# Performance work log

Measured on AMD Instinct MI355X. Metric: run time of the kernel, lower is better.

Reference implementation:

```python
import jax, jax.numpy as jnp
import numpy as np

WL = 5.32e-7      # wavelength (m)
DX = 8e-6         # pixel size (m)
N = 128           # image_size
L_COH = 2e-4      # coherence length used for training screens
DISTANCES = [0.0795, 0.0795, 0.106, 0.106]  # 3 inter-layer props + final prop (repeats last)


def _freq_grids():
    fx = jnp.fft.fftfreq(N, DX).astype(jnp.float32)
    FX, FY = jnp.meshgrid(fx, fx)  # 'xy' indexing, matches np.meshgrid default
    return FX, FY


def _prop_kernels():
    # Angular-spectrum transfer functions H(fx,fy) = exp(i*kz*z), evanescent cut.
    FX, FY = _freq_grids()
    k = 2.0 * np.pi / WL
    k2 = FX ** 2 + FY ** 2
    valid = (k2 <= (1.0 / WL) ** 2).astype(jnp.float32)
    kz = jnp.sqrt(jnp.maximum(k * k - k2 * valid, 0.0)) * valid
    return jnp.stack([jnp.exp(1j * kz * z) for z in DISTANCES]).astype(jnp.complex64)  # (4,N,N)


def _screens(c_noise):
    # Gaussian-Schell random screens T_m = fftshift(ifft2(C_m * sqrt(p(v)))) * H * W
    FX, FY = _freq_grids()
    v = jnp.sqrt(FX ** 2 + FY ** 2)
    p_v = 2.0 * np.pi * L_COH ** 2 * jnp.exp(-2.0 * (np.pi * L_COH * v) ** 2)
    C = (c_noise[..., 0] + 1j * c_noise[..., 1]).astype(jnp.complex64)  # (M,N,N)
    F_T = C * jnp.sqrt(p_v + 1e-12).astype(jnp.complex64)
    T = jnp.fft.fftshift(jnp.fft.ifft2(F_T), axes=(-2, -1)) * (N * N)
    return T  # (M,N,N) complex64


def setup_inputs() -> dict:
    key = jax.random.key(0)
    k1, k2, k3 = jax.random.split(key, 3)
    B, M = 32, 100
    x_in = jax.random.uniform(k1, (B, N, N), dtype=jnp.float32)
    phases = jax.random.uniform(k2, (3, N, N), dtype=jnp.float32) * (2.0 * np.pi)
    c_noise = jax.random.normal(k3, (M, N, N, 2), dtype=jnp.float32)
    return {"x_in": x_in, "phases": phases, "c_noise": c_noise, "M": M}


def reference(x_in, phases, c_noise, M):
    Hs = _prop_kernels()                # (4,N,N)
    T = _screens(c_noise[:M])           # (M,N,N)
    # field: (M,B,N,N) complex64 -- Monte-Carlo axis fully vectorized
    field = x_in.astype(jnp.complex64)[None, :, :, :] * T[:, None, :, :]
    for j in range(3):
        field = jnp.fft.ifft2(jnp.fft.fft2(field) * Hs[j])
        field = field * jnp.exp(1j * phases[j]).astype(jnp.complex64)
    field = jnp.fft.ifft2(jnp.fft.fft2(field) * Hs[3])
    intensity = jnp.sum(jnp.abs(field) ** 2, axis=(-2, -1))  # (M,B)
    return jnp.mean(intensity, axis=0)  # (B,)
```

## Files before the change

kernel.cpp:

```cpp
#include <hip/hip_runtime.h>
#include <hip/hip_fp16.h>


struct cplx { float x, y; };
__device__ __forceinline__ cplx cadd(cplx a, cplx b){ return {a.x+b.x, a.y+b.y}; }
__device__ __forceinline__ cplx csub(cplx a, cplx b){ return {a.x-b.x, a.y-b.y}; }
__device__ __forceinline__ cplx cmul(cplx a, cplx b){ return {a.x*b.x - a.y*b.y, a.x*b.y + a.y*b.x}; }
__device__ __forceinline__ cplx cmuli(cplx a){ return {-a.y, a.x}; }

__device__ __forceinline__ void idft4(cplx&A,cplx&B,cplx&C,cplx&D){
    cplx e0=cadd(A,C), e1=csub(A,C), o0=cadd(B,D), o1=csub(B,D);
    cplx i1 = cmuli(o1);
    A=cadd(e0,o0); B=cadd(e1,i1); C=csub(e0,o0); D=csub(e1,i1);
}
__device__ __forceinline__ void idft8(cplx a[8]){
    cplx e0=a[0],e1=a[2],e2=a[4],e3=a[6];
    cplx o0=a[1],o1=a[3],o2=a[5],o3=a[7];
    idft4(e0,e1,e2,e3); idft4(o0,o1,o2,o3);
    const float Ch = 0.70710678118654752f;
    cplx t1 = cmul(o1, cplx{ Ch, Ch});
    cplx t2 = cmuli(o2);
    cplx t3 = cmul(o3, cplx{-Ch, Ch});
    a[0]=cadd(e0,o0); a[4]=csub(e0,o0);
    a[1]=cadd(e1,t1); a[5]=csub(e1,t1);
    a[2]=cadd(e2,t2); a[6]=csub(e2,t2);
    a[3]=cadd(e3,t3); a[7]=csub(e3,t3);
}
__device__ __forceinline__ void idft16(cplx a[16]){
    cplx e[8]={a[0],a[2],a[4],a[6],a[8],a[10],a[12],a[14]};
    cplx o[8]={a[1],a[3],a[5],a[7],a[9],a[11],a[13],a[15]};
    idft8(e); idft8(o);
    const float Ch=0.70710678118654752f, c1=0.92387953251128674f, s1=0.38268343236508977f;
    const cplx w[8]={{1.f,0.f},{c1,s1},{Ch,Ch},{s1,c1},{0.f,1.f},{-s1,c1},{-Ch,Ch},{-c1,s1}};
    #pragma unroll
    for(int n=0;n<8;++n){ cplx t=cmul(o[n],w[n]); a[n]=cadd(e[n],t); a[n+8]=csub(e[n],t); }
}

#define LDSP 130
#define NR   16
#define MG   2

__device__ __forceinline__ void fft128_rows(cplx* fld, const cplx* tw, int tid)
{
    const int r = tid >> 3, t = tid & 7;
    cplx* row = fld + r * LDSP;
    {   cplx a[16];
        #pragma unroll
        for (int k1 = 0; k1 < 16; ++k1) a[k1] = row[t + 8*k1];
        idft16(a);
        #pragma unroll
        for (int n1 = 0; n1 < 16; ++n1) row[t + 8*n1] = cmul(a[n1], tw[(n1*t) & 127]);
    }
    __syncthreads();
    {   cplx b0[8], b1[8];
        #pragma unroll
        for (int k2 = 0; k2 < 8; ++k2) { b0[k2] = row[8*t + k2]; b1[k2] = row[8*(t+8) + k2]; }
        idft8(b0); idft8(b1);
        __syncthreads();
        #pragma unroll
        for (int n2 = 0; n2 < 8; ++n2) {
            row[ t      + 16*n2] = b0[n2];
            row[(t + 8) + 16*n2] = b1[n2];
        }
    }
    __syncthreads();
}

__device__ __forceinline__ unsigned h2_to_u(__half2 h){
    union { __half2 h; unsigned u; } v; v.h = h; return v.u;
}

__global__ __launch_bounds__(128)
void rowfft_kernel(const float* __restrict__ c_noise, __half2* __restrict__ mid,
                   float* __restrict__ Wsh)
{
    __shared__ cplx fld[NR * LDSP];
    __shared__ cplx tw[128];
    const int m   = blockIdx.x;
    const int rb  = blockIdx.y * NR;
    const int tid = threadIdx.x;

    if (m == 0) {
        float4* wz = (float4*)Wsh;
        #pragma unroll
        for (int k = 0; k < 4; ++k)
            wz[blockIdx.y*512 + k*128 + tid] = {0.f, 0.f, 0.f, 0.f};
    }

    {   float s, c;
        sincosf((float)tid * (float)(2.0 * M_PI / 128.0), &s, &c);
        tw[tid] = { c, s };
    }

    const float DF = 976.5625f;
    const float Ac = 2.5132741228718345e-7f;
    const float Bc = 7.8956835208714865e-7f;
    #pragma unroll
    for (int it = 0; it < NR; ++it) {
        const int i = rb + it, j = tid;
        float fi = (float)(((i+64)&127) - 64) * DF;
        float fj = (float)(((j+64)&127) - 64) * DF;
        float G  = sqrtf(Ac * expf(-Bc * (fi*fi + fj*fj)) + 1e-12f);
        float2 cv = ((const float2*)c_noise)[(size_t)m*16384 + i*128 + j];
        fld[it*LDSP + j] = { cv.x * G, cv.y * G };
    }
    __syncthreads();

    fft128_rows(fld, tw, tid);

    const int c = tid;
    uint4* dst4 = (uint4*)(mid + (size_t)m*16384 + (size_t)c*128 + rb);
    #pragma unroll
    for (int q = 0; q < 4; ++q) {
        uint4 pk;
        cplx v0 = fld[(4*q+0)*LDSP + c];
        cplx v1 = fld[(4*q+1)*LDSP + c];
        cplx v2 = fld[(4*q+2)*LDSP + c];
        cplx v3 = fld[(4*q+3)*LDSP + c];
        pk.x = h2_to_u(__floats2half2_rn(v0.x, v0.y));
        pk.y = h2_to_u(__floats2half2_rn(v1.x, v1.y));
        pk.z = h2_to_u(__floats2half2_rn(v2.x, v2.y));
        pk.w = h2_to_u(__floats2half2_rn(v3.x, v3.y));
        dst4[q] = pk;
    }
}

__global__ __launch_bounds__(256)
void colfft_acc_kernel(const __half2* __restrict__ mid,
                       float* __restrict__ Wsh, int M)
{
    __shared__ cplx fld[MG * NR * LDSP];
    __shared__ cplx tw[128];
    const int g   = blockIdx.x;
    const int cb  = blockIdx.y * NR;
    const int tid = threadIdx.x;
    const int grp = tid >> 7;
    const int lt  = tid & 127;

    if (tid < 128) {
        float s, c;
        sincosf((float)tid * (float)(2.0 * M_PI / 128.0), &s, &c);
        tw[tid] = { c, s };
    }

    {
        const int m = g*MG + grp;
        #pragma unroll
        for (int it = 0; it < NR; ++it) {
            float2 v = __half22float2(mid[(size_t)m*16384 + (size_t)(cb + it)*128 + lt]);
            fld[(grp*NR + it)*LDSP + lt] = { v.x, v.y };
        }
    }
    __syncthreads();

    fft128_rows(fld, tw, tid);

    #pragma unroll
    for (int it = 0; it < NR; ++it) {
        cplx v = fld[(grp*NR + it)*LDSP + lt];
        fld[(grp*NR + it)*LDSP + lt].x = v.x*v.x + v.y*v.y;
    }
    __syncthreads();

    const int c0 = cb ^ 64;
    #pragma unroll
    for (int k = 0; k < 8; ++k) {
        int v   = k*256 + tid;
        int lt2 = v >> 4, it = v & 15;
        float wv = fld[(       it)*LDSP + lt2].x
                 + fld[(NR  +  it)*LDSP + lt2].x;
        atomicAdd(&Wsh[((lt2 ^ 64) << 7) + c0 + it], wv);
    }
}

__global__ __launch_bounds__(256)
void dot_kernel(const float* __restrict__ x, const float* __restrict__ Wsh,
                float* __restrict__ out, int M)
{
    const int b = blockIdx.x;
    const float4* x4 = (const float4*)(x + (size_t)b * 16384);
    const float4* w4 = (const float4*)Wsh;
    float acc = 0.f;
    #pragma unroll 4
    for (int k = threadIdx.x; k < 4096; k += 256) {
        float4 xv = x4[k], wv = w4[k];
        acc = fmaf(xv.x*xv.x, wv.x, acc);
        acc = fmaf(xv.y*xv.y, wv.y, acc);
        acc = fmaf(xv.z*xv.z, wv.z, acc);
        acc = fmaf(xv.w*xv.w, wv.w, acc);
    }
    #pragma unroll
    for (int off = 32; off > 0; off >>= 1) acc += __shfl_down(acc, off);
    __shared__ float part[4];
    if ((threadIdx.x & 63) == 0) part[threadIdx.x >> 6] = acc;
    __syncthreads();
    if (threadIdx.x == 0)
        out[b] = (part[0] + part[1] + part[2] + part[3]) / (float)M;
}

extern "C" void kernel_launch(void* const* d_in, const int* in_sizes, int n_in,
                              void* d_out, int out_size, void* d_ws, size_t ws_size,
                              hipStream_t stream)
{
    (void)n_in; (void)ws_size;
    const float* x_in    = (const float*)d_in[0];
    const float* c_noise = (const float*)d_in[2];

    const int M = in_sizes[2] / (128*128*2);
    const int B = out_size;

    __half2* mid = (__half2*)d_ws;
    float*   Wsh = (float*)((char*)d_ws + (size_t)M*16384*sizeof(__half2));

    const int G = M / MG;

    rowfft_kernel    <<<dim3(M, 8), dim3(128), 0, stream>>>(c_noise, mid, Wsh);
    colfft_acc_kernel<<<dim3(G, 8), dim3(256), 0, stream>>>(mid, Wsh, M);
    dot_kernel       <<<dim3(B),    dim3(256), 0, stream>>>(x_in, Wsh,
                                                            (float*)d_out, M);
}
```

Before: 24.25 us.

## Rewrite column FFT as per-wavefront shuffle FFT accumulating over screen chunks

The column-FFT kernel no longer stages 16 columns for 2 screens in LDS and runs the shared-memory FFT. Each 64-lane wavefront now owns one column and computes a 128-point FFT in registers, using one radix-2 split and six __shfl_xor butterfly stages with precomputed twiddles. It loops over a chunk of 10 screens, accumulating |X|^2 in registers, then issues two bit-reversal-indexed atomics per lane. This removes LDS traffic, barriers and most atomics, but adds many cross-lane shuffles per screen, and the grid is now 32x10 blocks.

```diff
diff --git a/kernel.cpp b/kernel.cpp
--- a/kernel.cpp
+++ b/kernel.cpp
@@ -38,7 +38,7 @@
 
 #define LDSP 130
 #define NR   16
-#define MG   2
+#define CH   10
 
 __device__ __forceinline__ void fft128_rows(cplx* fld, const cplx* tw, int tid)
 {
@@ -129,48 +129,60 @@
 void colfft_acc_kernel(const __half2* __restrict__ mid,
                        float* __restrict__ Wsh, int M)
 {
-    __shared__ cplx fld[MG * NR * LDSP];
-    __shared__ cplx tw[128];
-    const int g   = blockIdx.x;
-    const int cb  = blockIdx.y * NR;
     const int tid = threadIdx.x;
-    const int grp = tid >> 7;
-    const int lt  = tid & 127;
-
-    if (tid < 128) {
-        float s, c;
-        sincosf((float)tid * (float)(2.0 * M_PI / 128.0), &s, &c);
-        tw[tid] = { c, s };
-    }
-
-    {
-        const int m = g*MG + grp;
-        #pragma unroll
-        for (int it = 0; it < NR; ++it) {
-            float2 v = __half22float2(mid[(size_t)m*16384 + (size_t)(cb + it)*128 + lt]);
-            fld[(grp*NR + it)*LDSP + lt] = { v.x, v.y };
+    const int w   = tid >> 6, l = tid & 63;
+    const int c   = blockIdx.x * 4 + w;
+    const int m0  = blockIdx.y * CH;
+    const int m1  = (m0 + CH < M) ? (m0 + CH) : M;
+
+    const float PI2 = 6.2831853071795865f;
+    float s1, c1; sincosf(PI2 * (float)l * (1.0f/128.0f), &s1, &c1);
+    float twr[6], twi[6];
+    const int spans[6] = {32, 16, 8, 4, 2, 1};
+    #pragma unroll
+    for (int k = 0; k < 6; ++k) {
+        const int s = spans[k];
+        if (l & s) {
+            float si, co;
+            sincosf(PI2 * (float)(l & (s-1)) / (float)(2*s), &si, &co);
+            twr[k] = co; twi[k] = si;
+        } else { twr[k] = 1.f; twi[k] = 0.f; }
+    }
+
+    float acc0 = 0.f, acc1 = 0.f;
+    #pragma unroll 2
+    for (int m = m0; m < m1; ++m) {
+        const __half2* col = mid + (size_t)m*16384 + (size_t)c*128;
+        float2 a = __half22float2(col[l]);
+        float2 b = __half22float2(col[l + 64]);
+
+        float r0 = a.x + b.x,  i0 = a.y + b.y;
+        float dr = a.x - b.x,  di = a.y - b.y;
+        float r1 = dr*c1 - di*s1, i1 = dr*s1 + di*c1;
+
+        #pragma unroll
+        for (int k = 0; k < 6; ++k) {
+            const int s = spans[k];
+            const bool hi = (l & s) != 0;
+            float pr, pi, d_r, d_i;
+            pr = __shfl_xor(r0, s); pi = __shfl_xor(i0, s);
+            d_r = hi ? (pr - r0) : (r0 + pr);
+            d_i = hi ? (pi - i0) : (i0 + pi);
+            r0 = d_r*twr[k] - d_i*twi[k]; i0 = d_r*twi[k] + d_i*twr[k];
+            pr = __shfl_xor(r1, s); pi = __shfl_xor(i1, s);
+            d_r = hi ? (pr - r1) : (r1 + pr);
+            d_i = hi ? (pi - i1) : (i1 + pi);
+            r1 = d_r*twr[k] - d_i*twi[k]; i1 = d_r*twi[k] + d_i*twr[k];
         }
-    }
-    __syncthreads();
-
-    fft128_rows(fld, tw, tid);
-
-    #pragma unroll
-    for (int it = 0; it < NR; ++it) {
-        cplx v = fld[(grp*NR + it)*LDSP + lt];
-        fld[(grp*NR + it)*LDSP + lt].x = v.x*v.x + v.y*v.y;
-    }
-    __syncthreads();
-
-    const int c0 = cb ^ 64;
-    #pragma unroll
-    for (int k = 0; k < 8; ++k) {
-        int v   = k*256 + tid;
-        int lt2 = v >> 4, it = v & 15;
-        float wv = fld[(       it)*LDSP + lt2].x
-                 + fld[(NR  +  it)*LDSP + lt2].x;
-        atomicAdd(&Wsh[((lt2 ^ 64) << 7) + c0 + it], wv);
-    }
+        acc0 += r0*r0 + i0*i0;
+        acc1 += r1*r1 + i1*i1;
+    }
+
+    const int rb   = ((l&1)<<5)|((l&2)<<3)|((l&4)<<1)|((l&8)>>1)|((l&16)>>3)|((l&32)>>5);
+    const int row0 = rb << 1, row1 = row0 | 1;
+    const int cs   = c ^ 64;
+    atomicAdd(&Wsh[((row0 ^ 64) << 7) + cs], acc0);
+    atomicAdd(&Wsh[((row1 ^ 64) << 7) + cs], acc1);
 }
 
 __global__ __launch_bounds__(256)
@@ -212,10 +224,10 @@
     __half2* mid = (__half2*)d_ws;
     float*   Wsh = (float*)((char*)d_ws + (size_t)M*16384*sizeof(__half2));
 
-    const int G = M / MG;
-
-    rowfft_kernel    <<<dim3(M, 8), dim3(128), 0, stream>>>(c_noise, mid, Wsh);
-    colfft_acc_kernel<<<dim3(G, 8), dim3(256), 0, stream>>>(mid, Wsh, M);
-    dot_kernel       <<<dim3(B),    dim3(256), 0, stream>>>(x_in, Wsh,
-                                                            (float*)d_out, M);
-}
+    const int chunks = (M + CH - 1) / CH;
+
+    rowfft_kernel    <<<dim3(M, 8),       dim3(128), 0, stream>>>(c_noise, mid, Wsh);
+    colfft_acc_kernel<<<dim3(32, chunks), dim3(256), 0, stream>>>(mid, Wsh, M);
+    dot_kernel       <<<dim3(B),          dim3(256), 0, stream>>>(x_in, Wsh,
+                                                                  (float*)d_out, M);
+}
```

Measured after the change: 33.33 us. +37.5%, slower.
